# Performance work log

Measured on AMD Instinct MI355X. Metric: run time of the kernel, lower is better.

The kernel has to match this reference:

```python
import jax, jax.numpy as jnp
import numpy as np

HIDDEN = 2048
HEADS = 16
KV_HEADS = 1
HEAD_DIM = 128
SEQ = 2048
BATCH = 1
LAM = 0.5


def _rotate_half(x):
    h = x.shape[-1] // 2
    return jnp.concatenate([-x[..., h:], x[..., :h]], axis=-1)


def _apply_rope(t, cos, sin):
    # t: [B,S,H,D], cos/sin: [S,D] -> broadcast over batch & heads
    c = cos[None, :, None, :]
    s = sin[None, :, None, :]
    return t * c + _rotate_half(t) * s


def setup_inputs() -> dict:
    key = jax.random.key(0)
    ks = jax.random.split(key, 8)
    x = jax.random.normal(ks[0], (BATCH, SEQ, HIDDEN), dtype=jnp.float32)
    # realistic RoPE tables, rotate-half layout: [S, D]
    inv_freq = 1.0 / (10000.0 ** (np.arange(0, HEAD_DIM, 2, dtype=np.float32) / HEAD_DIM))
    t = np.arange(SEQ, dtype=np.float32)
    ang = np.outer(t, inv_freq)                      # [S, D/2]
    ang = np.concatenate([ang, ang], axis=-1)        # [S, D]
    freqs_cos = jnp.asarray(np.cos(ang))
    freqs_sin = jnp.asarray(np.sin(ang))
    mask = jnp.tril(jnp.ones((SEQ, SEQ), dtype=bool))  # causal, True = attend
    scale = 1.0 / np.sqrt(HIDDEN)
    q1_w = jax.random.normal(ks[1], (HIDDEN, HEADS * HEAD_DIM), dtype=jnp.float32) * scale
    q2_w = jax.random.normal(ks[2], (HIDDEN, HEADS * HEAD_DIM), dtype=jnp.float32) * scale
    k_w = jax.random.normal(ks[3], (HIDDEN, KV_HEADS * HEAD_DIM), dtype=jnp.float32) * scale
    v_w = jax.random.normal(ks[4], (HIDDEN, KV_HEADS * HEAD_DIM), dtype=jnp.float32) * scale
    out_w = jax.random.normal(ks[5], (HEADS * HEAD_DIM, HIDDEN), dtype=jnp.float32) * scale
    return {"x": x, "freqs_cos": freqs_cos, "freqs_sin": freqs_sin, "mask": mask,
            "q1_w": q1_w, "q2_w": q2_w, "k_w": k_w, "v_w": v_w, "out_w": out_w}


def reference(x, freqs_cos, freqs_sin, mask, q1_w, q2_w, k_w, v_w, out_w):
    B, S, _ = x.shape
    q1 = (x @ q1_w).reshape(B, S, HEADS, HEAD_DIM)
    q2 = (x @ q2_w).reshape(B, S, HEADS, HEAD_DIM)
    k = (x @ k_w).reshape(B, S, KV_HEADS, HEAD_DIM)
    v = (x @ v_w).reshape(B, S, KV_HEADS, HEAD_DIM)
    q1 = _apply_rope(q1, freqs_cos, freqs_sin)
    q2 = _apply_rope(q2, freqs_cos, freqs_sin)
    k = _apply_rope(k, freqs_cos, freqs_sin)
    # MQA broadcast of the single KV head
    k = jnp.repeat(k, HEADS // KV_HEADS, axis=2)  # [B,S,H,D]
    v = jnp.repeat(v, HEADS // KV_HEADS, axis=2)
    inv_sqrt_d = 1.0 / jnp.sqrt(jnp.float32(HEAD_DIM))
    s1 = jnp.einsum('bqhd,bkhd->bhqk', q1, k) * inv_sqrt_d
    s2 = jnp.einsum('bqhd,bkhd->bhqk', q2, k) * inv_sqrt_d
    m = mask[None, None, :, :]
    neg = jnp.float32(-1e10)
    s1 = jnp.where(m, s1, neg)
    s2 = jnp.where(m, s2, neg)
    a1 = jax.nn.softmax(s1, axis=-1)
    a2 = jax.nn.softmax(s2, axis=-1)
    a = a1 - LAM * a2
    a = a / (jnp.sum(a, axis=-1, keepdims=True) + 1e-8)
    a = jnp.maximum(a, 0.0)
    out = jnp.einsum('bhqk,bkhd->bqhd', a, v).reshape(B, S, HEADS * HEAD_DIM)
    return out @ out_w
```

## Files before the change

### kernel.cpp

```cpp
#include <hip/hip_runtime.h>
#include <hip/hip_bf16.h>

typedef __attribute__((ext_vector_type(8))) short bf16x8;
typedef __attribute__((ext_vector_type(4))) float f32x4;

#define MFMA16(a, b, c) __builtin_amdgcn_mfma_f32_16x16x32_bf16((a), (b), (c), 0, 0, 0)

#define LDQ 4352
#define KSCALE 0.12751743f

__device__ __forceinline__ ushort f2bf(float f) {
    unsigned int x = __float_as_uint(f);
    x += 0x7fffu + ((x >> 16) & 1u);
    return (ushort)(x >> 16);
}
__device__ __forceinline__ float bf2f(ushort u) {
    return __uint_as_float(((unsigned int)u) << 16);
}
__device__ __forceinline__ float exp2_fast(float x) {
    float r;
    asm("v_exp_f32 %0, %1" : "=v"(r) : "v"(x));
    return r;
}
__device__ __forceinline__ unsigned int cvtpk(float lo, float hi) {
    unsigned int r;
    asm("v_cvt_pk_bf16_f32 %0, %1, %2" : "=v"(r) : "v"(lo), "v"(hi));
    return r;
}

__device__ __forceinline__ void gload16(const ushort* g, ushort* l) {
    __builtin_amdgcn_global_load_lds((const __attribute__((address_space(1))) unsigned int*)g,
                                     (__attribute__((address_space(3))) unsigned int*)l, 16, 0, 0);
}

__global__ __launch_bounds__(256) void prep_k(const float* __restrict__ x, ushort* __restrict__ xb,
                                              const float* __restrict__ q1w, const float* __restrict__ q2w,
                                              const float* __restrict__ kw, const float* __restrict__ vw,
                                              const float* __restrict__ ow,
                                              ushort* __restrict__ w1t, ushort* __restrict__ w2t,
                                              ushort* __restrict__ wkt, ushort* __restrict__ wvt,
                                              ushort* __restrict__ wot) {
    int bid = blockIdx.x;
    if (bid < 4096) {
        int i = bid * 256 + threadIdx.x;
        float4 v = ((const float4*)x)[i];
        ushort4 u;
        u.x = f2bf(v.x); u.y = f2bf(v.y); u.z = f2bf(v.z); u.w = f2bf(v.w);
        ((ushort4*)xb)[i] = u;
        return;
    }
    bid -= 4096;
    const float* in;
    ushort* out;
    int C, TX;
    if (bid < 4096) { in = q1w; out = w1t; C = 2048; TX = 64; }
    else if (bid < 8192) { bid -= 4096; in = q2w; out = w2t; C = 2048; TX = 64; }
    else if (bid < 12288) { bid -= 8192; in = ow; out = wot; C = 2048; TX = 64; }
    else if (bid < 12544) { bid -= 12288; in = kw; out = wkt; C = 128; TX = 4; }
    else { bid -= 12544; in = vw; out = wvt; C = 128; TX = 4; }
    __shared__ ushort t[32][33];
    const int c0 = (bid % TX) * 32, r0 = (bid / TX) * 32;
    const int lx = threadIdx.x & 31, ly = threadIdx.x >> 5;
#pragma unroll
    for (int i = 0; i < 4; ++i)
        t[ly + i * 8][lx] = f2bf(in[(size_t)(r0 + ly + i * 8) * C + c0 + lx]);
    __syncthreads();
    const int sc = threadIdx.x & 15;
    const int sr = threadIdx.x >> 4;
#pragma unroll
    for (int j = 0; j < 2; ++j) {
        const int cc = sr + j * 16;
        unsigned int w = (unsigned int)t[2 * sc][cc] | ((unsigned int)t[2 * sc + 1][cc] << 16);
        *(unsigned int*)&out[(size_t)(c0 + cc) * 2048 + r0 + 2 * sc] = w;
    }
}

template <bool FUSE>
__global__ __launch_bounds__(512) void gemm8_k(const ushort* __restrict__ A, int lda,
                                               const ushort* __restrict__ Bt, int ldb,
                                               void* __restrict__ C, int ldc,
                                               int K, int nbx, int cbf,
                                               const float* __restrict__ cs,
                                               const float* __restrict__ sn,
                                               ushort* __restrict__ vtb) {
    __shared__ ushort As[2 * 4096];
    __shared__ ushort Bs[2 * 4096];
    const int tid = threadIdx.x;
    const int lane = tid & 63, wid = tid >> 6;
    const int cpx = (int)gridDim.x >> 3;
    const int swz = ((int)blockIdx.x & 7) * cpx + ((int)blockIdx.x >> 3);
    const int nt = swz / nbx;
    const int m0 = (swz % nbx) * 128, n0 = nt * 128;
    const int wr = wid >> 2, wc = wid & 3;
    const int l15 = lane & 15, lhi = lane >> 4;

    const int srow = tid >> 2;
    const int scol = (((tid & 3) ^ ((srow >> 1) & 3)) << 3);
    const ushort* gA = A + (size_t)(m0 + srow) * lda + scol;
    const ushort* gB = Bt + (size_t)(n0 + srow) * ldb + scol;
    ushort* lA = &As[wid * 512];
    ushort* lB = &Bs[wid * 512];

    f32x4 acc[4][2];
#pragma unroll
    for (int m = 0; m < 4; ++m)
#pragma unroll
        for (int n = 0; n < 2; ++n) acc[m][n] = (f32x4){0.f, 0.f, 0.f, 0.f};

    const int fcol = (lhi << 4) ^ (((l15 >> 1) & 3) << 4);

    gload16(gA, lA);
    gload16(gB, lB);
    __syncthreads();

    int cur = 0;
    for (int k0 = 0; k0 < K; k0 += 32) {
        if (k0 + 32 < K) {
            gload16(gA + k0 + 32, lA + (cur ^ 1) * 4096);
            gload16(gB + k0 + 32, lB + (cur ^ 1) * 4096);
        }
        const char* aB = (const char*)&As[cur * 4096];
        const char* bB = (const char*)&Bs[cur * 4096];
        bf16x8 af[4], bfr[2];
#pragma unroll
        for (int m = 0; m < 4; ++m)
            af[m] = *(const bf16x8*)(aB + (wr * 64 + m * 16 + l15) * 64 + fcol);
#pragma unroll
        for (int n = 0; n < 2; ++n)
            bfr[n] = *(const bf16x8*)(bB + (wc * 16 + n * 64 + l15) * 64 + fcol);
#pragma unroll
        for (int m = 0; m < 4; ++m)
#pragma unroll
            for (int n = 0; n < 2; ++n)
                acc[m][n] = MFMA16(af[m], bfr[n], acc[m][n]);
        __syncthreads();
        cur ^= 1;
    }

    if (FUSE) {
        if (nt == 33) {
#pragma unroll
            for (int m = 0; m < 4; ++m) {
                const int rb = m0 + wr * 64 + m * 16 + lhi * 4;
#pragma unroll
                for (int n = 0; n < 2; ++n) {
                    const int d = wc * 16 + n * 64 + l15;
                    uint2 w;
                    w.x = cvtpk(acc[m][n][0], acc[m][n][1]);
                    w.y = cvtpk(acc[m][n][2], acc[m][n][3]);
                    *(uint2*)(vtb + (size_t)d * 2048 + rb) = w;
                }
            }
        } else {
            const float scale = (nt == 32) ? KSCALE : 1.0f;
            ushort* out = (ushort*)C;
            const int d0 = wc * 16 + l15;
#pragma unroll
            for (int m = 0; m < 4; ++m) {
                const int rb = m0 + wr * 64 + m * 16 + lhi * 4;
#pragma unroll
                for (int r = 0; r < 4; ++r) {
                    const int row = rb + r;
                    float c0 = cs[row * 128 + d0], c1 = cs[row * 128 + d0 + 64];
                    float s0 = sn[row * 128 + d0], s1 = sn[row * 128 + d0 + 64];
                    float t0 = acc[m][0][r], t1 = acc[m][1][r];
                    out[(size_t)row * ldc + n0 + d0] = f2bf((t0 * c0 - t1 * s0) * scale);
                    out[(size_t)row * ldc + n0 + d0 + 64] = f2bf((t1 * c1 + t0 * s1) * scale);
                }
            }
        }
    } else {
#pragma unroll
        for (int m = 0; m < 4; ++m) {
            const int rb = m0 + wr * 64 + m * 16 + lhi * 4;
#pragma unroll
            for (int n = 0; n < 2; ++n) {
                const int col = n0 + wc * 16 + n * 64 + l15;
#pragma unroll
                for (int r = 0; r < 4; ++r) {
                    if (cbf)
                        ((ushort*)C)[(size_t)(rb + r) * ldc + col] = f2bf(acc[m][n][r]);
                    else
                        ((float*)C)[(size_t)(rb + r) * ldc + col] = acc[m][n][r];
                }
            }
        }
    }
}


__device__ __forceinline__ void stage_k_chunk(const ushort* __restrict__ kb, int kc,
                                              ushort* __restrict__ kbuf, int wid, int lane) {
#pragma unroll
    for (int u = 0; u < 2; ++u) {
        const int w = wid * 2 + u;
        const int row = w * 4 + (lane >> 4);
        const int colb = ((lane & 15) * 16) ^ ((row & 7) << 4);
        gload16(kb + (size_t)(kc + row) * LDQ + (colb >> 1), kbuf + w * 512);
    }
}

__device__ __forceinline__ void stage_v_chunk(const ushort* __restrict__ vtb, int kc,
                                              ushort* __restrict__ vbuf, int wid, int lane) {
#pragma unroll
    for (int u = 0; u < 2; ++u) {
        const int w = wid * 2 + u;
        const int rowd = w * 16 + (lane >> 2);
        const int colb = ((lane & 3) * 16) ^ (((rowd >> 1) & 3) << 4);
        gload16(vtb + (size_t)rowd * 2048 + kc + (colb >> 1), vbuf + w * 512);
    }
}

__device__ __forceinline__ void load_k_frags(const ushort* __restrict__ kbuf, int l15, int lhi,
                                             bf16x8 kf[2][4]) {
    const char* kB = (const char*)kbuf;
#pragma unroll
    for (int n2 = 0; n2 < 2; ++n2) {
        const int r = n2 * 16 + l15;
#pragma unroll
        for (int c = 0; c < 4; ++c)
            kf[n2][c] = *(const bf16x8*)(kB + r * 256 + ((lhi * 16 + c * 64) ^ ((r & 7) << 4)));
    }
}

template <bool MASKED>
__device__ __forceinline__ void sums_chunk(const ushort* __restrict__ kbuf, int kc,
                                           int l15, int lhi, int qrow,
                                           const bf16x8* q1f, const bf16x8* q2f,
                                           float& sum1, float& sum2) {
    bf16x8 kf[2][4];
    load_k_frags(kbuf, l15, lhi, kf);
    f32x4 s1[2], s2[2];
#pragma unroll
    for (int n2 = 0; n2 < 2; ++n2) {
        s1[n2] = (f32x4){0.f, 0.f, 0.f, 0.f};
        s2[n2] = (f32x4){0.f, 0.f, 0.f, 0.f};
#pragma unroll
        for (int c = 0; c < 4; ++c) {
            s1[n2] = MFMA16(kf[n2][c], q1f[c], s1[n2]);
            s2[n2] = MFMA16(kf[n2][c], q2f[c], s2[n2]);
        }
    }
    const int kbase = kc + lhi * 4;
#pragma unroll
    for (int n2 = 0; n2 < 2; ++n2)
#pragma unroll
        for (int r = 0; r < 4; ++r) {
            float e1 = exp2_fast(s1[n2][r]);
            float e2 = exp2_fast(s2[n2][r]);
            if (MASKED) {
                bool ok = (kbase + n2 * 16 + r) <= qrow;
                e1 = ok ? e1 : 0.f;
                e2 = ok ? e2 : 0.f;
            }
            sum1 += e1;
            sum2 += e2;
        }
}

__global__ __launch_bounds__(256) void attn_sums_k(const ushort* __restrict__ qkv,
                                                   float* __restrict__ sums) {
    __shared__ ushort Kbuf[2 * 4096];
    const int bid = blockIdx.x;
    const int strip = 127 - (bid >> 3);
    const int cs = (bid >> 2) & 1;
    const int hg = bid & 3;
    const int q0 = strip << 4;
    const int lane = threadIdx.x & 63, wid = threadIdx.x >> 6;
    const int h = hg * 4 + wid;
    const int l15 = lane & 15, lhi = lane >> 4;
    const int qrow = q0 + l15;
    const ushort* kb = qkv + 4096;

    bf16x8 q1f[4], q2f[4];
    {
        size_t base = (size_t)qrow * LDQ + h * 128 + lhi * 8;
#pragma unroll
        for (int c = 0; c < 4; ++c) {
            q1f[c] = *(const bf16x8*)(qkv + base + c * 32);
            q2f[c] = *(const bf16x8*)(qkv + base + 2048 + c * 32);
        }
    }

    const int nchunk = (strip >> 1) + 1;
    const int ndiag = nchunk - 1;
    const int nch = (nchunk - cs + 1) >> 1;

    float sum1 = 0.f, sum2 = 0.f;
    if (nch > 0) stage_k_chunk(kb, cs * 32, Kbuf, wid, lane);
    __syncthreads();
    for (int i = 0; i < nch; ++i) {
        const int ch = cs + 2 * i, kc = ch << 5;
        if (i + 1 < nch) stage_k_chunk(kb, kc + 64, Kbuf + ((i + 1) & 1) * 4096, wid, lane);
        const ushort* kcur = Kbuf + (i & 1) * 4096;
        if (ch == ndiag)
            sums_chunk<true>(kcur, kc, l15, lhi, qrow, q1f, q2f, sum1, sum2);
        else
            sums_chunk<false>(kcur, kc, l15, lhi, qrow, q1f, q2f, sum1, sum2);
        __syncthreads();
    }

    sum1 += __shfl_xor(sum1, 16);
    sum1 += __shfl_xor(sum1, 32);
    sum2 += __shfl_xor(sum2, 16);
    sum2 += __shfl_xor(sum2, 32);

    if (lhi == 0) {
        sums[(size_t)((cs * 2 + 0) * 16 + h) * 2048 + qrow] = sum1;
        sums[(size_t)((cs * 2 + 1) * 16 + h) * 2048 + qrow] = sum2;
    }
}

template <bool MASKED>
__device__ __forceinline__ void pv_chunk(const ushort* __restrict__ kbuf, const ushort* __restrict__ vbuf,
                                         int kc, ushort* __restrict__ Pb,
                                         int l15, int lhi, int qrow,
                                         const bf16x8* q1f, const bf16x8* q2f,
                                         float c1, float c2, f32x4* o) {
    bf16x8 kf[2][4];
    load_k_frags(kbuf, l15, lhi, kf);
    bf16x8 vf[8];
    const char* vB = (const char*)vbuf;
#pragma unroll
    for (int dt = 0; dt < 8; ++dt) {
        const int d = dt * 16 + l15;
        vf[dt] = *(const bf16x8*)(vB + d * 64 + ((lhi * 16) ^ (((d >> 1) & 3) << 4)));
    }
    f32x4 s1[2], s2[2];
#pragma unroll
    for (int n2 = 0; n2 < 2; ++n2) {
        s1[n2] = (f32x4){0.f, 0.f, 0.f, 0.f};
        s2[n2] = (f32x4){0.f, 0.f, 0.f, 0.f};
#pragma unroll
        for (int c = 0; c < 4; ++c) {
            s1[n2] = MFMA16(kf[n2][c], q1f[c], s1[n2]);
            s2[n2] = MFMA16(kf[n2][c], q2f[c], s2[n2]);
        }
    }
    const int kbase = kc + lhi * 4;
#pragma unroll
    for (int n2 = 0; n2 < 2; ++n2) {
        float p[4];
#pragma unroll
        for (int r = 0; r < 4; ++r) {
            float e1 = exp2_fast(s1[n2][r]) * c1;
            float e2 = exp2_fast(s2[n2][r]) * c2;
            float pv = fmaxf(e1 - e2, 0.f);
            if (MASKED) pv = ((kbase + n2 * 16 + r) <= qrow) ? pv : 0.f;
            p[r] = pv;
        }
        uint2 w;
        w.x = cvtpk(p[0], p[1]);
        w.y = cvtpk(p[2], p[3]);
        *(uint2*)(Pb + l15 * 40 + n2 * 16 + lhi * 4) = w;
    }
    asm volatile("s_waitcnt lgkmcnt(0)" ::: "memory");
    bf16x8 pf = *(const bf16x8*)(Pb + l15 * 40 + lhi * 8);
#pragma unroll
    for (int dt = 0; dt < 8; ++dt)
        o[dt] = MFMA16(pf, vf[dt], o[dt]);
}

__global__ __launch_bounds__(256) void attn_pv_k(const ushort* __restrict__ qkv,
                                                 const ushort* __restrict__ vtb,
                                                 const float* __restrict__ sums,
                                                 ushort* __restrict__ op0,
                                                 ushort* __restrict__ op1) {
    __shared__ ushort Kbuf[2 * 4096];
    __shared__ ushort Vbuf[2 * 4096];
    __shared__ ushort P[4][16][40];
    const int bid = blockIdx.x;
    const int strip = 127 - (bid >> 3);
    const int cs = (bid >> 2) & 1;
    const int hg = bid & 3;
    const int q0 = strip << 4;
    const int lane = threadIdx.x & 63, wid = threadIdx.x >> 6;
    const int h = hg * 4 + wid;
    const int l15 = lane & 15, lhi = lane >> 4;
    const int qrow = q0 + l15;
    const ushort* kb = qkv + 4096;

    bf16x8 q1f[4], q2f[4];
    {
        size_t base = (size_t)qrow * LDQ + h * 128 + lhi * 8;
#pragma unroll
        for (int c = 0; c < 4; ++c) {
            q1f[c] = *(const bf16x8*)(qkv + base + c * 32);
            q2f[c] = *(const bf16x8*)(qkv + base + 2048 + c * 32);
        }
    }

    const float sum1 = sums[(size_t)(0 * 16 + h) * 2048 + qrow] + sums[(size_t)(2 * 16 + h) * 2048 + qrow];
    const float sum2 = sums[(size_t)(1 * 16 + h) * 2048 + qrow] + sums[(size_t)(3 * 16 + h) * 2048 + qrow];
    const float inv_denom = 1.0f / (0.5f + 1e-8f);
    const float c1 = inv_denom / sum1;
    const float c2 = 0.5f * inv_denom / sum2;

    f32x4 o[8];
#pragma unroll
    for (int dt = 0; dt < 8; ++dt) o[dt] = (f32x4){0.f, 0.f, 0.f, 0.f};

    const int nchunk = (strip >> 1) + 1;
    const int ndiag = nchunk - 1;
    const int nch = (nchunk - cs + 1) >> 1;

    if (nch > 0) {
        stage_k_chunk(kb, cs * 32, Kbuf, wid, lane);
        stage_v_chunk(vtb, cs * 32, Vbuf, wid, lane);
    }
    __syncthreads();
    for (int i = 0; i < nch; ++i) {
        const int ch = cs + 2 * i, kc = ch << 5;
        if (i + 1 < nch) {
            stage_k_chunk(kb, kc + 64, Kbuf + ((i + 1) & 1) * 4096, wid, lane);
            stage_v_chunk(vtb, kc + 64, Vbuf + ((i + 1) & 1) * 4096, wid, lane);
        }
        const ushort* kcur = Kbuf + (i & 1) * 4096;
        const ushort* vcur = Vbuf + (i & 1) * 4096;
        ushort* Pb = &P[wid][0][0];
        if (ch == ndiag)
            pv_chunk<true>(kcur, vcur, kc, Pb, l15, lhi, qrow, q1f, q2f, c1, c2, o);
        else
            pv_chunk<false>(kcur, vcur, kc, Pb, l15, lhi, qrow, q1f, q2f, c1, c2, o);
        __syncthreads();
    }

    ushort* op = cs ? op1 : op0;
#pragma unroll
    for (int dt = 0; dt < 8; ++dt)
#pragma unroll
        for (int r = 0; r < 4; ++r)
            op[(size_t)(q0 + lhi * 4 + r) * 2048 + h * 128 + dt * 16 + l15] = f2bf(o[dt][r]);
}

__device__ __forceinline__ unsigned int addbf2(unsigned int a, unsigned int b) {
    float alo = bf2f((ushort)a), ahi = bf2f((ushort)(a >> 16));
    float blo = bf2f((ushort)b), bhi = bf2f((ushort)(b >> 16));
    return (unsigned int)f2bf(alo + blo) | ((unsigned int)f2bf(ahi + bhi) << 16);
}
__global__ void combine_k(const ushort* __restrict__ o0, const ushort* __restrict__ o1,
                          ushort* __restrict__ out, int n8) {
    int i = blockIdx.x * blockDim.x + threadIdx.x;
    if (i >= n8) return;
    uint4 a = ((const uint4*)o0)[i];
    uint4 b = ((const uint4*)o1)[i];
    uint4 c;
    c.x = addbf2(a.x, b.x);
    c.y = addbf2(a.y, b.y);
    c.z = addbf2(a.z, b.z);
    c.w = addbf2(a.w, b.w);
    ((uint4*)out)[i] = c;
}

extern "C" void kernel_launch(void* const* d_in, const int* in_sizes, int n_in,
                              void* d_out, int out_size, void* d_ws, size_t ws_size,
                              hipStream_t stream) {
    const int S = 2048, HID = 2048;

    const float* x = (const float*)d_in[0];
    const float* fcos = (const float*)d_in[1];
    const float* fsin = (const float*)d_in[2];
    const float* q1w = (const float*)d_in[4];
    const float* q2w = (const float*)d_in[5];
    const float* kw = (const float*)d_in[6];
    const float* vw = (const float*)d_in[7];
    const float* ow = (const float*)d_in[8];

    ushort* xb = (ushort*)d_ws;
    ushort* btq = xb + (size_t)4194304;
    ushort* w1t = btq;
    ushort* w2t = btq + (size_t)2048 * 2048;
    ushort* wkt = btq + (size_t)4096 * 2048;
    ushort* wvt = btq + (size_t)4224 * 2048;
    ushort* wot = btq + (size_t)8912896;
    ushort* qkvb = wot + (size_t)4194304;
    ushort* vtb = qkvb + (size_t)8912896;
    float* sums = (float*)(vtb + (size_t)262144);
    ushort* opart0 = xb;
    ushort* opart1 = w1t;
    ushort* aob = w2t;

    prep_k<<<dim3(16896), dim3(256), 0, stream>>>(x, xb, q1w, q2w, kw, vw, ow,
                                                  w1t, w2t, wkt, wvt, wot);

    gemm8_k<true><<<dim3(544), dim3(512), 0, stream>>>(xb, HID, btq, HID, qkvb, LDQ, HID, 16, 1,
                                                       fcos, fsin, vtb);

    attn_sums_k<<<dim3(1024), dim3(256), 0, stream>>>(qkvb, sums);

    attn_pv_k<<<dim3(1024), dim3(256), 0, stream>>>(qkvb, vtb, sums, opart0, opart1);

    combine_k<<<dim3(2048), dim3(256), 0, stream>>>(opart0, opart1, aob, S * HID / 8);

    gemm8_k<false><<<dim3(256), dim3(512), 0, stream>>>(aob, HID, wot, HID, (float*)d_out, HID, HID, 16, 0,
                                                        nullptr, nullptr, nullptr);
}
```

Measured before the change: 179.3 us.

## Use 256x256 tiled QKV GEMM kernel with fused RoPE and V-transpose epilogue

Replaces the 128x128-tile fused QKV projection GEMM with a dedicated kernel that uses 256x256 tiles, a 64-wide K step, XOR-swizzled LDS staging, and explicit barrier/waitcnt scheduling. The next tile's prefetch is interleaved with MFMA phases. Larger tiles raise arithmetic intensity and cut global/LDS traffic per FLOP. The cost is only 136 blocks, fewer than the CU count, and much higher register and LDS usage (128 KB shared), which lowers occupancy.

```diff
diff --git a/kernel.cpp b/kernel.cpp
--- a/kernel.cpp
+++ b/kernel.cpp
@@ -75,14 +75,130 @@
     }
 }
 
-template <bool FUSE>
+__global__ __launch_bounds__(512) void gemmqkv_k(const ushort* __restrict__ A, int lda,
+                                                 const ushort* __restrict__ Bt, int ldb,
+                                                 ushort* __restrict__ C, int ldc,
+                                                 int K, int nbx,
+                                                 const float* __restrict__ cs,
+                                                 const float* __restrict__ sn,
+                                                 ushort* __restrict__ vtb) {
+    __shared__ ushort As[2 * 16384];
+    __shared__ ushort Bs[2 * 16384];
+    const int tid = threadIdx.x;
+    const int lane = tid & 63, wid = tid >> 6;
+    const int cpx = (int)gridDim.x >> 3;
+    const int swz = ((int)blockIdx.x & 7) * cpx + ((int)blockIdx.x >> 3);
+    const int nt = swz / nbx;
+    const int m0 = (swz % nbx) * 256, n0 = nt * 256;
+    const int wr = wid >> 2, wc = wid & 3;
+    const int l15 = lane & 15, lhi = lane >> 4;
+
+    const int strow = lane >> 3;
+    const int stcol = ((lane & 7) ^ strow) << 3;
+
+    f32x4 acc[8][4];
+#pragma unroll
+    for (int m = 0; m < 8; ++m)
+#pragma unroll
+        for (int n = 0; n < 4; ++n) acc[m][n] = (f32x4){0.f, 0.f, 0.f, 0.f};
+
+    const int rsw = (l15 & 7) << 4;
+
+    const int NT = K >> 6;
+
+#pragma unroll
+    for (int q = 0; q < 4; ++q) {
+        const int r0 = q * 64 + wid * 8;
+        gload16(A + (size_t)(m0 + r0 + strow) * lda + stcol, &As[r0 * 64]);
+        gload16(Bt + (size_t)(n0 + r0 + strow) * ldb + stcol, &Bs[r0 * 64]);
+    }
+    asm volatile("s_waitcnt vmcnt(0)" ::: "memory");
+    __syncthreads();
+
+    int cur = 0;
+    for (int kt = 0; kt < NT; ++kt) {
+        const char* aB = (const char*)&As[cur * 16384];
+        const char* bB = (const char*)&Bs[cur * 16384];
+#pragma unroll
+        for (int p = 0; p < 4; ++p) {
+            const int mg = p >> 1, ks = p & 1;
+            bf16x8 af[4], bfr[4];
+#pragma unroll
+            for (int i = 0; i < 4; ++i) {
+                const int row = wr * 128 + (mg * 4 + i) * 16 + l15;
+                af[i] = *(const bf16x8*)(aB + row * 128 + ((ks * 64 + lhi * 16) ^ rsw));
+            }
+#pragma unroll
+            for (int n = 0; n < 4; ++n) {
+                const int row = wc * 16 + n * 64 + l15;
+                bfr[n] = *(const bf16x8*)(bB + row * 128 + ((ks * 64 + lhi * 16) ^ rsw));
+            }
+            if (p == 0 && kt + 1 < NT) {
+                const int kc2 = (kt + 1) * 64;
+                ushort* An = &As[(cur ^ 1) * 16384];
+                ushort* Bn = &Bs[(cur ^ 1) * 16384];
+#pragma unroll
+                for (int q = 0; q < 4; ++q) {
+                    const int r0 = q * 64 + wid * 8;
+                    gload16(A + (size_t)(m0 + r0 + strow) * lda + kc2 + stcol, An + r0 * 64);
+                    gload16(Bt + (size_t)(n0 + r0 + strow) * ldb + kc2 + stcol, Bn + r0 * 64);
+                }
+            }
+            if (p == 3)
+                asm volatile("s_waitcnt vmcnt(0)" ::: "memory");
+            __builtin_amdgcn_s_barrier();
+            asm volatile("s_waitcnt lgkmcnt(0)" ::: "memory");
+            __builtin_amdgcn_sched_barrier(0);
+#pragma unroll
+            for (int i = 0; i < 4; ++i)
+#pragma unroll
+                for (int n = 0; n < 4; ++n)
+                    acc[mg * 4 + i][n] = MFMA16(af[i], bfr[n], acc[mg * 4 + i][n]);
+            __builtin_amdgcn_s_barrier();
+        }
+        cur ^= 1;
+    }
+
+#pragma unroll
+    for (int pair = 0; pair < 2; ++pair) {
+        if (nt == 16 && pair == 1) {
+#pragma unroll
+            for (int n = 2; n < 4; ++n) {
+                const int d = wc * 16 + (n - 2) * 64 + l15;
+#pragma unroll
+                for (int m = 0; m < 8; ++m) {
+                    const int rb = m0 + wr * 128 + m * 16 + lhi * 4;
+                    uint2 w;
+                    w.x = cvtpk(acc[m][n][0], acc[m][n][1]);
+                    w.y = cvtpk(acc[m][n][2], acc[m][n][3]);
+                    *(uint2*)(vtb + (size_t)d * 2048 + rb) = w;
+                }
+            }
+        } else {
+            const float scale = (nt == 16) ? KSCALE : 1.0f;
+            const int d0 = wc * 16 + l15;
+            const int colb = n0 + pair * 128 + d0;
+#pragma unroll
+            for (int m = 0; m < 8; ++m) {
+                const int rb = m0 + wr * 128 + m * 16 + lhi * 4;
+#pragma unroll
+                for (int r = 0; r < 4; ++r) {
+                    const int row = rb + r;
+                    float c0 = cs[row * 128 + d0], c1v = cs[row * 128 + d0 + 64];
+                    float s0 = sn[row * 128 + d0], s1v = sn[row * 128 + d0 + 64];
+                    float t0 = acc[m][pair * 2 + 0][r], t1 = acc[m][pair * 2 + 1][r];
+                    C[(size_t)row * ldc + colb] = f2bf((t0 * c0 - t1 * s0) * scale);
+                    C[(size_t)row * ldc + colb + 64] = f2bf((t1 * c1v + t0 * s1v) * scale);
+                }
+            }
+        }
+    }
+}
+
 __global__ __launch_bounds__(512) void gemm8_k(const ushort* __restrict__ A, int lda,
                                                const ushort* __restrict__ Bt, int ldb,
                                                void* __restrict__ C, int ldc,
-                                               int K, int nbx, int cbf,
-                                               const float* __restrict__ cs,
-                                               const float* __restrict__ sn,
-                                               ushort* __restrict__ vtb) {
+                                               int K, int nbx, int cbf) {
     __shared__ ushort As[2 * 4096];
     __shared__ ushort Bs[2 * 4096];
     const int tid = threadIdx.x;
@@ -137,52 +253,18 @@
         cur ^= 1;
     }
 
-    if (FUSE) {
-        if (nt == 33) {
-#pragma unroll
-            for (int m = 0; m < 4; ++m) {
-                const int rb = m0 + wr * 64 + m * 16 + lhi * 4;
-#pragma unroll
-                for (int n = 0; n < 2; ++n) {
-                    const int d = wc * 16 + n * 64 + l15;
-                    uint2 w;
-                    w.x = cvtpk(acc[m][n][0], acc[m][n][1]);
-                    w.y = cvtpk(acc[m][n][2], acc[m][n][3]);
-                    *(uint2*)(vtb + (size_t)d * 2048 + rb) = w;
-                }
-            }
-        } else {
-            const float scale = (nt == 32) ? KSCALE : 1.0f;
-            ushort* out = (ushort*)C;
-            const int d0 = wc * 16 + l15;
-#pragma unroll
-            for (int m = 0; m < 4; ++m) {
-                const int rb = m0 + wr * 64 + m * 16 + lhi * 4;
-#pragma unroll
-                for (int r = 0; r < 4; ++r) {
-                    const int row = rb + r;
-                    float c0 = cs[row * 128 + d0], c1 = cs[row * 128 + d0 + 64];
-                    float s0 = sn[row * 128 + d0], s1 = sn[row * 128 + d0 + 64];
-                    float t0 = acc[m][0][r], t1 = acc[m][1][r];
-                    out[(size_t)row * ldc + n0 + d0] = f2bf((t0 * c0 - t1 * s0) * scale);
-                    out[(size_t)row * ldc + n0 + d0 + 64] = f2bf((t1 * c1 + t0 * s1) * scale);
-                }
-            }
-        }
-    } else {
-#pragma unroll
-        for (int m = 0; m < 4; ++m) {
-            const int rb = m0 + wr * 64 + m * 16 + lhi * 4;
-#pragma unroll
-            for (int n = 0; n < 2; ++n) {
-                const int col = n0 + wc * 16 + n * 64 + l15;
-#pragma unroll
-                for (int r = 0; r < 4; ++r) {
-                    if (cbf)
-                        ((ushort*)C)[(size_t)(rb + r) * ldc + col] = f2bf(acc[m][n][r]);
-                    else
-                        ((float*)C)[(size_t)(rb + r) * ldc + col] = acc[m][n][r];
-                }
+#pragma unroll
+    for (int m = 0; m < 4; ++m) {
+        const int rb = m0 + wr * 64 + m * 16 + lhi * 4;
+#pragma unroll
+        for (int n = 0; n < 2; ++n) {
+            const int col = n0 + wc * 16 + n * 64 + l15;
+#pragma unroll
+            for (int r = 0; r < 4; ++r) {
+                if (cbf)
+                    ((ushort*)C)[(size_t)(rb + r) * ldc + col] = f2bf(acc[m][n][r]);
+                else
+                    ((float*)C)[(size_t)(rb + r) * ldc + col] = acc[m][n][r];
             }
         }
     }
@@ -483,8 +565,8 @@
     prep_k<<<dim3(16896), dim3(256), 0, stream>>>(x, xb, q1w, q2w, kw, vw, ow,
                                                   w1t, w2t, wkt, wvt, wot);
 
-    gemm8_k<true><<<dim3(544), dim3(512), 0, stream>>>(xb, HID, btq, HID, qkvb, LDQ, HID, 16, 1,
-                                                       fcos, fsin, vtb);
+    gemmqkv_k<<<dim3(136), dim3(512), 0, stream>>>(xb, HID, btq, HID, qkvb, LDQ, HID, 8,
+                                                   fcos, fsin, vtb);
 
     attn_sums_k<<<dim3(1024), dim3(256), 0, stream>>>(qkvb, sums);
 
@@ -492,6 +574,5 @@
 
     combine_k<<<dim3(2048), dim3(256), 0, stream>>>(opart0, opart1, aob, S * HID / 8);
 
-    gemm8_k<false><<<dim3(256), dim3(512), 0, stream>>>(aob, HID, wot, HID, (float*)d_out, HID, HID, 16, 0,
-                                                        nullptr, nullptr, nullptr);
-}
+    gemm8_k<<<dim3(256), dim3(512), 0, stream>>>(aob, HID, wot, HID, (float*)d_out, HID, HID, 16, 0);
+}
```

Measured after the change: 197.8 us. +10.4%, slower.
